# Optimization experiments

Measured on AMD Instinct MI355X. Metric: run time of the kernel, lower is better.

The kernel has to match this reference:

```python
import jax, jax.numpy as jnp
import numpy as np

DIM, WIDTH, TOTAL, BATCH, NSLOTS = 4096, 4, 16384, 8, 256


def setup_inputs() -> dict:
    key = jax.random.key(0)
    ks = jax.random.split(key, 6)
    x = jax.random.normal(ks[0], (DIM, TOTAL), dtype=jnp.float32)
    weight = jax.random.normal(ks[1], (DIM, WIDTH), dtype=jnp.float32) * 0.1
    conv_states = jax.random.normal(ks[2], (NSLOTS, DIM, WIDTH - 1), dtype=jnp.float32)
    cuts = jnp.sort(jax.random.randint(ks[3], (BATCH - 1,), 1, TOTAL)).astype(jnp.int32)
    query_start_loc = jnp.concatenate([
        jnp.zeros((1,), jnp.int32), cuts, jnp.full((1,), TOTAL, jnp.int32)])
    cache_indices = jax.random.permutation(ks[4], NSLOTS)[:BATCH].astype(jnp.int32)
    initial_state_mode = jax.random.randint(ks[5], (BATCH,), 0, 2).astype(jnp.int32)
    return dict(x=x, weight=weight, conv_states=conv_states,
                query_start_loc=query_start_loc, cache_indices=cache_indices,
                initial_state_mode=initial_state_mode,
                pad_slot_id=-1, residual_connection=1)


def _causal_conv1d_varlen(x, weight, conv_states, qsl, cache_indices, init_mode,
                          pad_slot_id, residual_connection):
    dim, T = x.shape
    width = weight.shape[1]
    state_len = width - 1
    nslots = conv_states.shape[0]
    B = qsl.shape[0] - 1

    t = jnp.arange(T)
    # sequence id and local position of every packed token
    seg = jnp.clip(jnp.searchsorted(qsl, t, side='right') - 1, 0, B - 1)  # [T]
    p = t - qsl[seg]                                                      # [T] local pos
    raw_slot = cache_indices[seg]
    valid_slot = raw_slot != pad_slot_id
    slot = jnp.where(valid_slot, raw_slot, 0)
    use_init = (init_mode[seg] != 0) & valid_slot                         # [T]

    # depthwise causal conv: out[:,t] = sum_k w[:,k] * concat(init_state, x_seq)[:, p+k]
    out = jnp.zeros_like(x)
    for k in range(width):
        d = width - 1 - k  # lookback distance
        if d == 0:
            val = x
        else:
            in_seq = p >= d
            vx = x[:, jnp.clip(t - d, 0, T - 1)]                          # [dim,T]
            st_idx = jnp.clip(state_len - d + p, 0, state_len - 1)        # [T]
            vs = conv_states[slot, :, st_idx].T                           # [dim,T]
            val = jnp.where(in_seq[None, :], vx,
                            jnp.where(use_init[None, :], vs, 0.0))
        out = out + weight[:, k:k + 1] * val

    if residual_connection:
        out = out + x

    # updated cache: last state_len entries of concat(init_state, x_seq) per sequence
    j = jnp.arange(state_len)                                             # [S]
    start, end = qsl[:-1], qsl[1:]
    L = end - start                                                       # [B]
    gx = end[:, None] + j[None, :] - state_len                            # [B,S] global idx
    from_x = gx >= start[:, None]                                         # [B,S]
    sidx = jnp.clip(L[:, None] + j[None, :], 0, state_len - 1)            # [B,S]
    b_valid = cache_indices != pad_slot_id
    b_slot = jnp.where(b_valid, cache_indices, 0)
    b_init = (init_mode != 0) & b_valid
    vx_new = x[:, jnp.clip(gx, 0, T - 1)]                                 # [dim,B,S]
    vs_new = jnp.transpose(conv_states[b_slot[:, None], :, sidx], (2, 0, 1))  # [dim,B,S]
    init_vals = jnp.where(b_init[None, :, None], vs_new, 0.0)
    new_states = jnp.where(from_x[None, :, :], vx_new, init_vals)         # [dim,B,S]
    new_states = jnp.transpose(new_states, (1, 0, 2))                     # [B,dim,S]

    # scatter (pad_slot_id rows go to a throwaway extra slot)
    cs_ext = jnp.concatenate(
        [conv_states, jnp.zeros((1, dim, state_len), conv_states.dtype)], axis=0)
    scatter_idx = jnp.where(b_valid, cache_indices, nslots)
    cs_ext = cs_ext.at[scatter_idx].set(new_states)
    return out, cs_ext[:nslots]


def reference(x, weight, conv_states, query_start_loc, cache_indices,
              initial_state_mode, pad_slot_id, residual_connection):
    return _causal_conv1d_varlen(x, weight, conv_states, query_start_loc,
                                 cache_indices, initial_state_mode,
                                 pad_slot_id, residual_connection)
```

## Files before the change

kernel.cpp:

```cpp
#include <hip/hip_runtime.h>

#define DIM 4096
#define TOTAL 16384
#define WIDTH 4
#define STATE_LEN 3
#define BATCH 8
#define NSLOTS 256
#define TVEC (TOTAL / 4)

__global__ __launch_bounds__(256) void conv_out_kernel(
    const float* __restrict__ x, const float* __restrict__ weight,
    const float* __restrict__ cs, const int* __restrict__ qsl,
    const int* __restrict__ cache_indices, const int* __restrict__ init_mode,
    const int* __restrict__ pad_p, const int* __restrict__ res_p,
    float* __restrict__ out)
{
    __shared__ int s_qsl[BATCH + 1];
    __shared__ int s_ci[BATCH];
    __shared__ int s_im[BATCH];
    __shared__ int s_pad, s_res;
    if (threadIdx.x < BATCH + 1) s_qsl[threadIdx.x] = qsl[threadIdx.x];
    if (threadIdx.x >= 32 && threadIdx.x < 32 + BATCH) s_ci[threadIdx.x - 32] = cache_indices[threadIdx.x - 32];
    if (threadIdx.x >= 64 && threadIdx.x < 64 + BATCH) s_im[threadIdx.x - 64] = init_mode[threadIdx.x - 64];
    if (threadIdx.x == 96) s_pad = pad_p[0];
    if (threadIdx.x == 97) s_res = res_p[0];
    __syncthreads();

    unsigned v = blockIdx.x * 256u + threadIdx.x;
    int d  = v >> 12;
    int tv = v & (TVEC - 1);
    int t0 = tv << 2;

    const float4* xr = (const float4*)(x + (size_t)d * TOTAL);
    float4 cur = xr[tv];
    float4 prev = make_float4(0.f, 0.f, 0.f, 0.f);
    if (tv > 0) prev = xr[tv - 1];
    float win[7] = {prev.y, prev.z, prev.w, cur.x, cur.y, cur.z, cur.w};

    float4 w = ((const float4*)weight)[d];

    int seg = 0;
    while (seg + 1 < BATCH && t0 >= s_qsl[seg + 1]) seg++;

    float res[4];
    #pragma unroll
    for (int i = 0; i < 4; i++) {
        int t = t0 + i;
        while (seg + 1 < BATCH && t >= s_qsl[seg + 1]) seg++;
        int p = t - s_qsl[seg];
        float xt = win[3 + i];
        float acc;
        if (p >= 3) {
            acc = w.x * win[i] + w.y * win[i + 1] + w.z * win[i + 2] + w.w * xt;
        } else {
            int raw = s_ci[seg];
            bool valid = (raw != s_pad);
            int slot = valid ? raw : 0;
            bool use_init = valid && (s_im[seg] != 0);
            const float* csrow = cs + ((size_t)slot * DIM + d) * STATE_LEN;
            float xm1 = (p >= 1) ? win[i + 2] : (use_init ? csrow[2 + p] : 0.f);
            float xm2 = (p >= 2) ? win[i + 1] : (use_init ? csrow[1 + p] : 0.f);
            float xm3 =                          (use_init ? csrow[0 + p] : 0.f);
            acc = w.x * xm3 + w.y * xm2 + w.z * xm1 + w.w * xt;
        }
        if (s_res) acc += xt;
        res[i] = acc;
    }
    ((float4*)(out + (size_t)d * TOTAL))[tv] = make_float4(res[0], res[1], res[2], res[3]);
}

__global__ __launch_bounds__(256) void state_update_kernel(
    const float* __restrict__ x, const float* __restrict__ cs,
    const int* __restrict__ qsl, const int* __restrict__ cache_indices,
    const int* __restrict__ init_mode, const int* __restrict__ pad_p,
    float* __restrict__ out_states)
{
    int idx = blockIdx.x * blockDim.x + threadIdx.x;
    if (idx >= BATCH * DIM) return;
    int b = idx >> 12;
    int d = idx & (DIM - 1);
    int pad = pad_p[0];
    int raw = cache_indices[b];
    if (raw == pad) return;
    int start = qsl[b], end = qsl[b + 1];
    int L = end - start;
    bool init = (init_mode[b] != 0);
    const float* xrow  = x + (size_t)d * TOTAL;
    const float* csrow = cs + ((size_t)raw * DIM + d) * STATE_LEN;
    float*       orow  = out_states + ((size_t)raw * DIM + d) * STATE_LEN;
    #pragma unroll
    for (int j = 0; j < STATE_LEN; j++) {
        int gx = end + j - STATE_LEN;
        float val;
        if (gx >= start) {
            val = xrow[gx];
        } else if (init) {
            int sidx = L + j;
            if (sidx < 0) sidx = 0;
            if (sidx > STATE_LEN - 1) sidx = STATE_LEN - 1;
            val = csrow[sidx];
        } else {
            val = 0.f;
        }
        orow[j] = val;
    }
}

extern "C" void kernel_launch(void* const* d_in, const int* in_sizes, int n_in,
                              void* d_out, int out_size, void* d_ws, size_t ws_size,
                              hipStream_t stream) {
    const float* x      = (const float*)d_in[0];
    const float* weight = (const float*)d_in[1];
    const float* cs     = (const float*)d_in[2];
    const int*   qsl    = (const int*)d_in[3];
    const int*   ci     = (const int*)d_in[4];
    const int*   im     = (const int*)d_in[5];
    const int*   pad    = (const int*)d_in[6];
    const int*   res    = (const int*)d_in[7];

    float* out        = (float*)d_out;
    float* out_states = out + (size_t)DIM * TOTAL;

    hipMemcpyAsync(out_states, cs, (size_t)NSLOTS * DIM * STATE_LEN * sizeof(float),
                   hipMemcpyDeviceToDevice, stream);

    conv_out_kernel<<<(DIM * TVEC) / 256, 256, 0, stream>>>(
        x, weight, cs, qsl, ci, im, pad, res, out);

    state_update_kernel<<<(BATCH * DIM + 255) / 256, 256, 0, stream>>>(
        x, cs, qsl, ci, im, pad, out_states);
}
```

Baseline: 503.8 us.

## Fuse conv output, state copy and state update into one kernel launch

Merges the device memcpy of conv_states, the conv output kernel and the state update kernel into a single launch. Extra blocks copy the state array and overwrite slots touched by the batch, using a shared slot-to-batch map. Residual addition is folded into the last weight, and stores use nontemporal hints. This removes two launches and the separate copy pass, but the state path now does strided scalar gathers from x inside float4 writes.

```diff
diff --git a/kernel.cpp b/kernel.cpp
--- a/kernel.cpp
+++ b/kernel.cpp
@@ -7,102 +7,120 @@
 #define BATCH 8
 #define NSLOTS 256
 #define TVEC (TOTAL / 4)
+#define NCONV_BLK ((DIM * TVEC) / 256)
+#define SROW (DIM * STATE_LEN)
+#define S4_PER_SLOT (SROW / 4)
+#define NSTATE4 (NSLOTS * S4_PER_SLOT)
+#define NSTATE_BLK (NSTATE4 / 256)
 
-__global__ __launch_bounds__(256) void conv_out_kernel(
+typedef float floatx4 __attribute__((ext_vector_type(4)));
+
+__global__ __launch_bounds__(256) void fused_kernel(
     const float* __restrict__ x, const float* __restrict__ weight,
     const float* __restrict__ cs, const int* __restrict__ qsl,
     const int* __restrict__ cache_indices, const int* __restrict__ init_mode,
     const int* __restrict__ pad_p, const int* __restrict__ res_p,
-    float* __restrict__ out)
+    float* __restrict__ out, float* __restrict__ out_states)
 {
     __shared__ int s_qsl[BATCH + 1];
     __shared__ int s_ci[BATCH];
     __shared__ int s_im[BATCH];
+    __shared__ int s_map[NSLOTS];
     __shared__ int s_pad, s_res;
-    if (threadIdx.x < BATCH + 1) s_qsl[threadIdx.x] = qsl[threadIdx.x];
-    if (threadIdx.x >= 32 && threadIdx.x < 32 + BATCH) s_ci[threadIdx.x - 32] = cache_indices[threadIdx.x - 32];
-    if (threadIdx.x >= 64 && threadIdx.x < 64 + BATCH) s_im[threadIdx.x - 64] = init_mode[threadIdx.x - 64];
-    if (threadIdx.x == 96) s_pad = pad_p[0];
-    if (threadIdx.x == 97) s_res = res_p[0];
-    __syncthreads();
 
-    unsigned v = blockIdx.x * 256u + threadIdx.x;
-    int d  = v >> 12;
-    int tv = v & (TVEC - 1);
-    int t0 = tv << 2;
+    if (blockIdx.x < NCONV_BLK) {
+        if (threadIdx.x < BATCH + 1) s_qsl[threadIdx.x] = qsl[threadIdx.x];
+        if (threadIdx.x >= 32 && threadIdx.x < 32 + BATCH) s_ci[threadIdx.x - 32] = cache_indices[threadIdx.x - 32];
+        if (threadIdx.x >= 64 && threadIdx.x < 64 + BATCH) s_im[threadIdx.x - 64] = init_mode[threadIdx.x - 64];
+        if (threadIdx.x == 96) s_pad = pad_p[0];
+        if (threadIdx.x == 97) s_res = res_p[0];
+        __syncthreads();
 
-    const float4* xr = (const float4*)(x + (size_t)d * TOTAL);
-    float4 cur = xr[tv];
-    float4 prev = make_float4(0.f, 0.f, 0.f, 0.f);
-    if (tv > 0) prev = xr[tv - 1];
-    float win[7] = {prev.y, prev.z, prev.w, cur.x, cur.y, cur.z, cur.w};
+        unsigned v = blockIdx.x * 256u + threadIdx.x;
+        int d  = v >> 12;
+        int tv = v & (TVEC - 1);
+        int t0 = tv << 2;
 
-    float4 w = ((const float4*)weight)[d];
+        const floatx4* xr = (const floatx4*)(x + (size_t)d * TOTAL);
+        floatx4 cur = xr[tv];
+        floatx4 prev = (floatx4){0.f, 0.f, 0.f, 0.f};
+        if (tv > 0) prev = xr[tv - 1];
+        float win[7] = {prev.y, prev.z, prev.w, cur.x, cur.y, cur.z, cur.w};
 
-    int seg = 0;
-    while (seg + 1 < BATCH && t0 >= s_qsl[seg + 1]) seg++;
+        floatx4 w = ((const floatx4*)weight)[d];
+        if (s_res) w.w += 1.0f;
 
-    float res[4];
-    #pragma unroll
-    for (int i = 0; i < 4; i++) {
-        int t = t0 + i;
-        while (seg + 1 < BATCH && t >= s_qsl[seg + 1]) seg++;
-        int p = t - s_qsl[seg];
-        float xt = win[3 + i];
-        float acc;
-        if (p >= 3) {
-            acc = w.x * win[i] + w.y * win[i + 1] + w.z * win[i + 2] + w.w * xt;
+        int seg = 0;
+        float res4[4];
+        #pragma unroll
+        for (int i = 0; i < 4; i++) {
+            int t = t0 + i;
+            while (seg + 1 < BATCH && t >= s_qsl[seg + 1]) seg++;
+            int p = t - s_qsl[seg];
+            float xt = win[3 + i];
+            float acc;
+            if (p >= 3) {
+                acc = w.x * win[i] + w.y * win[i + 1] + w.z * win[i + 2] + w.w * xt;
+            } else {
+                int raw = s_ci[seg];
+                bool valid = (raw != s_pad);
+                int slot = valid ? raw : 0;
+                bool use_init = valid && (s_im[seg] != 0);
+                const float* csrow = cs + ((size_t)slot * DIM + d) * STATE_LEN;
+                float xm1 = (p >= 1) ? win[i + 2] : (use_init ? csrow[2 + p] : 0.f);
+                float xm2 = (p >= 2) ? win[i + 1] : (use_init ? csrow[1 + p] : 0.f);
+                float xm3 =                          (use_init ? csrow[0 + p] : 0.f);
+                acc = w.x * xm3 + w.y * xm2 + w.z * xm1 + w.w * xt;
+            }
+            res4[i] = acc;
+        }
+        floatx4 rv = (floatx4){res4[0], res4[1], res4[2], res4[3]};
+        __builtin_nontemporal_store(rv, (floatx4*)(out + (size_t)d * TOTAL) + tv);
+    } else {
+        s_map[threadIdx.x] = -1;
+        if (threadIdx.x < BATCH + 1) s_qsl[threadIdx.x] = qsl[threadIdx.x];
+        if (threadIdx.x >= 32 && threadIdx.x < 32 + BATCH) s_im[threadIdx.x - 32] = init_mode[threadIdx.x - 32];
+        __syncthreads();
+        if (threadIdx.x < BATCH) {
+            int raw = cache_indices[threadIdx.x];
+            if (raw != pad_p[0] && raw >= 0 && raw < NSLOTS) s_map[raw] = threadIdx.x;
+        }
+        __syncthreads();
+
+        int f = (blockIdx.x - NCONV_BLK) * 256 + threadIdx.x;
+        int slot = f / S4_PER_SLOT;
+        int r4   = f - slot * S4_PER_SLOT;
+        int b = s_map[slot];
+        floatx4 cv = ((const floatx4*)cs)[f];
+        if (b < 0) {
+            __builtin_nontemporal_store(cv, (floatx4*)out_states + f);
         } else {
-            int raw = s_ci[seg];
-            bool valid = (raw != s_pad);
-            int slot = valid ? raw : 0;
-            bool use_init = valid && (s_im[seg] != 0);
-            const float* csrow = cs + ((size_t)slot * DIM + d) * STATE_LEN;
-            float xm1 = (p >= 1) ? win[i + 2] : (use_init ? csrow[2 + p] : 0.f);
-            float xm2 = (p >= 2) ? win[i + 1] : (use_init ? csrow[1 + p] : 0.f);
-            float xm3 =                          (use_init ? csrow[0 + p] : 0.f);
-            acc = w.x * xm3 + w.y * xm2 + w.z * xm1 + w.w * xt;
+            int start = s_qsl[b], end = s_qsl[b + 1];
+            int L = end - start;
+            bool init = (s_im[b] != 0);
+            int base = r4 * 4;
+            float r[4];
+            #pragma unroll
+            for (int e = 0; e < 4; e++) {
+                int idx = base + e;
+                int d = idx / 3;
+                int j = idx - d * 3;
+                int gx = end + j - STATE_LEN;
+                float val;
+                if (gx >= start) {
+                    val = x[(size_t)d * TOTAL + gx];
+                } else if (init) {
+                    int sidx = L + j;
+                    if (sidx > STATE_LEN - 1) sidx = STATE_LEN - 1;
+                    val = cs[(size_t)slot * SROW + (idx - j) + sidx];
+                } else {
+                    val = 0.f;
+                }
+                r[e] = val;
+            }
+            floatx4 rv = (floatx4){r[0], r[1], r[2], r[3]};
+            __builtin_nontemporal_store(rv, (floatx4*)out_states + f);
         }
-        if (s_res) acc += xt;
-        res[i] = acc;
-    }
-    ((float4*)(out + (size_t)d * TOTAL))[tv] = make_float4(res[0], res[1], res[2], res[3]);
-}
-
-__global__ __launch_bounds__(256) void state_update_kernel(
-    const float* __restrict__ x, const float* __restrict__ cs,
-    const int* __restrict__ qsl, const int* __restrict__ cache_indices,
-    const int* __restrict__ init_mode, const int* __restrict__ pad_p,
-    float* __restrict__ out_states)
-{
-    int idx = blockIdx.x * blockDim.x + threadIdx.x;
-    if (idx >= BATCH * DIM) return;
-    int b = idx >> 12;
-    int d = idx & (DIM - 1);
-    int pad = pad_p[0];
-    int raw = cache_indices[b];
-    if (raw == pad) return;
-    int start = qsl[b], end = qsl[b + 1];
-    int L = end - start;
-    bool init = (init_mode[b] != 0);
-    const float* xrow  = x + (size_t)d * TOTAL;
-    const float* csrow = cs + ((size_t)raw * DIM + d) * STATE_LEN;
-    float*       orow  = out_states + ((size_t)raw * DIM + d) * STATE_LEN;
-    #pragma unroll
-    for (int j = 0; j < STATE_LEN; j++) {
-        int gx = end + j - STATE_LEN;
-        float val;
-        if (gx >= start) {
-            val = xrow[gx];
-        } else if (init) {
-            int sidx = L + j;
-            if (sidx < 0) sidx = 0;
-            if (sidx > STATE_LEN - 1) sidx = STATE_LEN - 1;
-            val = csrow[sidx];
-        } else {
-            val = 0.f;
-        }
-        orow[j] = val;
     }
 }
 
@@ -121,12 +139,6 @@
     float* out        = (float*)d_out;
     float* out_states = out + (size_t)DIM * TOTAL;
 
-    hipMemcpyAsync(out_states, cs, (size_t)NSLOTS * DIM * STATE_LEN * sizeof(float),
-                   hipMemcpyDeviceToDevice, stream);
-
-    conv_out_kernel<<<(DIM * TVEC) / 256, 256, 0, stream>>>(
-        x, weight, cs, qsl, ci, im, pad, res, out);
-
-    state_update_kernel<<<(BATCH * DIM + 255) / 256, 256, 0, stream>>>(
-        x, cs, qsl, ci, im, pad, out_states);
+    fused_kernel<<<NCONV_BLK + NSTATE_BLK, 256, 0, stream>>>(
+        x, weight, cs, qsl, ci, im, pad, res, out, out_states);
 }
```

Result: no change. 499.4 us (-0.9%).
